# Performance work log

Hardware: AMD Instinct MI355X
Metric: run time of the kernel (lower is better)

The kernel has to match this reference:

```python
import jax, jax.numpy as jnp
import numpy as np
import math

B, S, D = 2, 2048, 1024
H, HKV = 16, 4
HD = D // H
NREP = H // HKV
E, TOPK, SHARED = 8, 2, 1
HIDDEN = 684
AUX_COEF = 0.01
RMS_EPS = 1e-5


def setup_inputs() -> dict:
    key = jax.random.key(0)
    ks = jax.random.split(key, 14)
    def w(k, shape):
        return jax.random.normal(k, shape, jnp.float32) * 0.02
    # standard RoPE angles, base 10000
    t = jnp.arange(S, dtype=jnp.float32)
    inv = 1.0 / (10000.0 ** (jnp.arange(0, HD, 2, dtype=jnp.float32) / HD))
    ang = t[:, None] * inv[None, :]  # [S, HD//2]
    return {
        "x": jax.random.normal(ks[0], (B, S, D), jnp.float32),
        "freqs_cos": jnp.cos(ang),
        "freqs_sin": jnp.sin(ang),
        "wq": w(ks[1], (D, D)),
        "wk": w(ks[2], (D, HKV * HD)),
        "wv": w(ks[3], (D, HKV * HD)),
        "wo": w(ks[4], (D, D)),
        "router_w": w(ks[5], (D, E)),
        "ew1": w(ks[6], (E, D, HIDDEN)),
        "ew2": w(ks[7], (E, HIDDEN, D)),
        "ew3": w(ks[8], (E, D, HIDDEN)),
        "sw1": w(ks[9], (SHARED, D, HIDDEN)),
        "sw2": w(ks[10], (SHARED, HIDDEN, D)),
        "sw3": w(ks[11], (SHARED, D, HIDDEN)),
        "g_attn": jnp.ones((D,), jnp.float32),
        "g_ffn": jnp.ones((D,), jnp.float32),
        "start_pos": 0,
    }


def rmsnorm(x, g, eps=RMS_EPS):
    xf = x.astype(jnp.float32)
    n = xf * jax.lax.rsqrt(jnp.mean(xf * xf, axis=-1, keepdims=True) + eps)
    return g * n.astype(x.dtype)


def rope(x, cos, sin):
    # pairs are consecutive elements (view_as_complex of reshape(..., -1, 2))
    xr, xi = x[..., 0::2], x[..., 1::2]
    c = cos[None, :, None, :]  # [1,S,1,HD//2]
    s = sin[None, :, None, :]
    r = xr * c - xi * s
    i = xr * s + xi * c
    return jnp.stack([r, i], axis=-1).reshape(x.shape)


def attention(x, freqs_cos, freqs_sin, wq, wk, wv, wo):
    b, s, d = x.shape
    q = (x @ wq).reshape(b, s, H, HD)
    k = (x @ wk).reshape(b, s, HKV, HD)
    v = (x @ wv).reshape(b, s, HKV, HD)
    q = rope(q, freqs_cos, freqs_sin)
    k = rope(k, freqs_cos, freqs_sin)
    k = jnp.repeat(k, NREP, axis=2)
    v = jnp.repeat(v, NREP, axis=2)
    q, k, v = (t.transpose(0, 2, 1, 3) for t in (q, k, v))  # [B,H,S,HD]
    att = jnp.einsum('bhqd,bhkd->bhqk', q, k) * (1.0 / math.sqrt(HD))
    # faithful to torch: tril then masked_fill(att == 0, -inf)
    tri = jnp.tril(jnp.ones((s, s), bool))
    att = jnp.where(tri, att, 0.0)
    att = jnp.where(att == 0.0, -jnp.inf, att)
    att = jax.nn.softmax(att, axis=-1)
    out = jnp.einsum('bhqk,bhkd->bhqd', att, v)
    out = out.transpose(0, 2, 1, 3).reshape(b, s, d)
    return out @ wo


def moe(x, router_w, ew1, ew2, ew3, sw1, sw2, sw3):
    b, s, d = x.shape
    xf = x.reshape(-1, d)                       # [N, D]
    logits = xf @ router_w                      # [N, E]
    probs = jax.nn.softmax(logits, axis=-1)
    _, topk_idx = jax.lax.top_k(logits, TOPK)   # [N, K]
    topk_p, _ = jax.lax.top_k(probs, TOPK)      # same ordering (softmax monotone)
    density = jnp.mean(jax.nn.one_hot(topk_idx[:, 0], E, dtype=jnp.float32), axis=0)
    aux = AUX_COEF * jnp.sum(density * jnp.mean(probs, axis=0)) * E
    # per-token combine weight over experts [N, E]
    onehot = jax.nn.one_hot(topk_idx, E, dtype=xf.dtype)  # [N, K, E]
    cw = jnp.einsum('nk,nke->ne', topk_p, onehot)
    # dense expert evaluation (jit-friendly dispatch/combine equivalent)
    h = jax.nn.silu(jnp.einsum('nd,edh->neh', xf, ew1)) * jnp.einsum('nd,edh->neh', xf, ew3)
    eo = jnp.einsum('neh,ehd->ned', h, ew2)
    out = jnp.einsum('ne,ned->nd', cw, eo)
    for i in range(SHARED):
        out = out + (jax.nn.silu(xf @ sw1[i]) * (xf @ sw3[i])) @ sw2[i]
    return out.reshape(b, s, d), aux


def reference(x, freqs_cos, freqs_sin, wq, wk, wv, wo, router_w, ew1, ew2, ew3, sw1, sw2, sw3, g_attn, g_ffn, start_pos):
    h = x + attention(rmsnorm(x, g_attn), freqs_cos, freqs_sin, wq, wk, wv, wo)
    ffn_out, aux = moe(rmsnorm(h, g_ffn), router_w, ew1, ew2, ew3, sw1, sw2, sw3)
    return h + ffn_out, aux
```

## Files before the change

kernel.cpp:

```cpp
#include <hip/hip_runtime.h>
#include <hip/hip_bf16.h>
#include <cstdint>

#define B_ 2
#define S_ 2048
#define D_ 1024
#define H_ 16
#define HKV_ 4
#define HD_ 64
#define E_ 8
#define HIDDEN_ 684
#define NT_ (B_*S_)
#define NEGBIG (-1e30f)

using bf16 = __hip_bfloat16;
typedef __attribute__((ext_vector_type(8))) short short8v;
typedef __attribute__((ext_vector_type(4))) short short4v;
typedef __attribute__((ext_vector_type(4))) float f32x4;

static __device__ __forceinline__ float b2f(bf16 v){ return __bfloat162float(v); }
static __device__ __forceinline__ bf16 f2b(float v){ return __float2bfloat16(v); }
static __device__ __forceinline__ short f2bs(float v){ bf16 h = f2b(v); return *reinterpret_cast<short*>(&h); }
static __device__ __forceinline__ float dload(const void* p, size_t i, int isbf){
  return isbf ? b2f(((const bf16*)p)[i]) : ((const float*)p)[i];
}

__global__ void k_detect(const uint32_t* __restrict__ g, int* __restrict__ flag, int* __restrict__ cnt){
  if(threadIdx.x == 0 && blockIdx.x == 0){
    uint32_t w0 = g[0], w1 = g[1], w2 = g[2], w3 = g[3];
    int bf;
    if(w0==0x3F803F80u && w1==0x3F803F80u && w2==0x3F803F80u && w3==0x3F803F80u) bf = 1;
    else if(w0==0x3F800000u && w1==0x3F800000u && w2==0x3F800000u && w3==0x3F800000u) bf = 0;
    else bf = 1;
    flag[0] = bf;
  }
  if(threadIdx.x < E_ && blockIdx.x == 0) cnt[threadIdx.x] = 0;
}

__global__ __launch_bounds__(256) void k_rms(const void* __restrict__ X, const void* __restrict__ g,
                                             bf16* __restrict__ outb, float* __restrict__ outf,
                                             const int* __restrict__ flag, int xdyn){
  int isbf = flag[0]; int xb = xdyn ? isbf : 0;
  int t = blockIdx.x; int tid = threadIdx.x;
  float v[4]; float ss = 0.f;
  #pragma unroll
  for(int i=0;i<4;i++){ v[i] = dload(X, (size_t)t*D_ + tid + i*256, xb); ss += v[i]*v[i]; }
  __shared__ float red[256];
  red[tid] = ss; __syncthreads();
  for(int st=128; st>0; st>>=1){ if(tid<st) red[tid] += red[tid+st]; __syncthreads(); }
  float r = rsqrtf(red[0]*(1.f/(float)D_) + 1e-5f);
  #pragma unroll
  for(int i=0;i<4;i++){
    int d = tid + i*256;
    float val = v[i]*r*dload(g, d, isbf);
    outb[(size_t)t*D_ + d] = f2b(val);
    if(outf) outf[(size_t)t*D_ + d] = val;
  }
}

#define ASTRIDE 40

static __device__ __forceinline__ f32x4 mfma16(short8v a, short8v b, f32x4 c){
  return __builtin_amdgcn_mfma_f32_16x16x32_bf16(a, b, c, 0, 0, 0);
}

template<int AMAP, int OMODE>
__global__ __launch_bounds__(256) void k_mgemm(
    const bf16* __restrict__ A, const void* __restrict__ Bw, void* __restrict__ Cout,
    const void* __restrict__ resid,
    int M, int N, int K, int ldc,
    const int* __restrict__ cnt, const int* __restrict__ offs, const int* __restrict__ list,
    const int* __restrict__ flag)
{
  int isbf = flag[0];
  int e, ct, rt;
  int base = 0; size_t eoff = 0;
  if(cnt){
    e = blockIdx.x;
    int nc = (N+63)>>6;
    ct = blockIdx.y % nc; rt = blockIdx.y / nc;
    M = cnt[e]; if(M<0) M=0; if(M>NT_) M=NT_;
    base = offs[e];
    eoff = (size_t)e*(size_t)K*(size_t)N;
  } else {
    e = 0; ct = blockIdx.x; rt = blockIdx.y;
  }
  int m0 = rt*128; if(m0 >= M) return;
  int n0 = ct*64;

  __shared__ short As[2][128*ASTRIDE];
  __shared__ short Bs[2][64*ASTRIDE];
  __shared__ int rowA[128];

  int tid = threadIdx.x;
  int w = tid>>6, l = tid&63, lr = l&15, lg = l>>4;

  if(tid < 128){
    int rloc = m0 + tid;
    int ar = -1;
    if(rloc < M) ar = (AMAP==2) ? (list[e*NT_ + rloc]>>1) : (base + rloc);
    rowA[tid] = ar;
  }
  __syncthreads();

  int srow = tid>>1, skh = (tid&1)*16;
  int keya = (srow>>4)&3, kb0 = skh>>3;
  int bk = tid>>3, bnc = (tid&7)*8;
  int keyb = ((tid&7)>>1)&3;
  int bcol = (((bk>>3)^keyb)<<3) + (bk&7);
  int arow = rowA[srow];

  short8v rA0, rA1, rB;

  auto loadAB = [&](int kt){
    int k0 = kt*32;
    {
      short tmp[16];
      if(arow >= 0 && k0+skh+16 <= K){
        const short4v* src = (const short4v*)(A + (size_t)arow*K + k0 + skh);
        #pragma unroll
        for(int c=0;c<4;c++) *(short4v*)&tmp[c*4] = src[c];
      } else {
        #pragma unroll
        for(int i=0;i<16;i++){
          int gk = k0+skh+i;
          short v = 0;
          if(arow>=0 && gk<K) v = *(const short*)&A[(size_t)arow*K+gk];
          tmp[i] = v;
        }
      }
      #pragma unroll
      for(int i=0;i<8;i++){ rA0[i]=tmp[i]; rA1[i]=tmp[8+i]; }
    }
    {
      int gk = k0 + bk;
      short tmp[8];
      if(gk < K && n0+bnc+8 <= N){
        size_t bb = eoff + (size_t)gk*N + n0 + bnc;
        if(isbf){
          const short4v* src = (const short4v*)((const bf16*)Bw + bb);
          *(short4v*)&tmp[0] = src[0];
          *(short4v*)&tmp[4] = src[1];
        } else {
          const f32x4* src = (const f32x4*)((const float*)Bw + bb);
          f32x4 f0 = src[0], f1 = src[1];
          #pragma unroll
          for(int i=0;i<4;i++){ tmp[i]=f2bs(f0[i]); tmp[4+i]=f2bs(f1[i]); }
        }
      } else {
        #pragma unroll
        for(int i=0;i<8;i++){
          int gn = n0+bnc+i;
          float v = 0.f;
          if(gk<K && gn<N) v = dload(Bw, eoff + (size_t)gk*N + gn, isbf);
          tmp[i] = f2bs(v);
        }
      }
      #pragma unroll
      for(int i=0;i<8;i++) rB[i]=tmp[i];
    }
  };
  auto writeAB = [&](int buf){
    *(short8v*)&As[buf][srow*ASTRIDE + ((kb0^keya)<<3)]     = rA0;
    *(short8v*)&As[buf][srow*ASTRIDE + (((kb0+1)^keya)<<3)] = rA1;
    #pragma unroll
    for(int i=0;i<8;i++) Bs[buf][(bnc+i)*ASTRIDE + bcol] = rB[i];
  };

  f32x4 acc[2][4] = {};
  int KT = (K+31)>>5;

  loadAB(0); writeAB(0);
  __syncthreads();
  int cur = 0;
  for(int kt=0; kt<KT; ++kt){
    bool more = (kt+1 < KT);
    if(more) loadAB(kt+1);
    short8v a[2], b[4];
    #pragma unroll
    for(int fi=0;fi<2;fi++)
      a[fi] = *(const short8v*)&As[cur][(w*32+fi*16+lr)*ASTRIDE + ((lg^((w*2+fi)&3))<<3)];
    #pragma unroll
    for(int fj=0;fj<4;fj++)
      b[fj] = *(const short8v*)&Bs[cur][(fj*16+lr)*ASTRIDE + ((lg^fj)<<3)];
    #pragma unroll
    for(int fi=0;fi<2;fi++)
      #pragma unroll
      for(int fj=0;fj<4;fj++)
        acc[fi][fj] = mfma16(a[fi], b[fj], acc[fi][fj]);
    if(more){ writeAB(cur^1); cur ^= 1; }
    __syncthreads();
  }

  #pragma unroll
  for(int fi=0;fi<2;fi++){
    #pragma unroll
    for(int r=0;r<4;r++){
      int rl = m0 + w*32 + fi*16 + lg*4 + r;
      if(rl >= M) continue;
      int orow;
      if(OMODE==2){ orow = list[e*NT_ + rl]; if(orow<0||orow>=2*NT_) continue; }
      else orow = base + rl;
      #pragma unroll
      for(int fj=0;fj<4;fj++){
        int gcol = n0 + fj*16 + lr;
        if(gcol >= N) continue;
        float v = acc[fi][fj][r];
        size_t o = (size_t)orow*ldc + gcol;
        if(OMODE==1)      ((float*)Cout)[o] = v + dload(resid, o, isbf);
        else if(OMODE==2) ((bf16*)Cout)[o] = f2b(v);
        else if(OMODE==3) ((float*)Cout)[o] = ((float*)Cout)[o] + v;
        else              ((bf16*)Cout)[o] = f2b(v);
      }
    }
  }
}

__global__ __launch_bounds__(256) void k_qkv(
    const bf16* __restrict__ A, const void* __restrict__ Wq, const void* __restrict__ Wk,
    const void* __restrict__ Wv, bf16* __restrict__ Oq, bf16* __restrict__ Ok, bf16* __restrict__ Ov,
    const void* __restrict__ fc, const void* __restrict__ fs,
    const int* __restrict__ flag)
{
  int isbf = flag[0];
  int ct = blockIdx.x, rt = blockIdx.y;
  const void* Bw; bf16* Cout; int N, n0;
  if(ct < 16){ Bw = Wq; Cout = Oq; N = D_;  n0 = ct*64; }
  else if(ct < 20){ Bw = Wk; Cout = Ok; N = 256; n0 = (ct-16)*64; }
  else { Bw = Wv; Cout = Ov; N = 256; n0 = (ct-20)*64; }
  const int K = D_, M = NT_;
  int m0 = rt*128;
  int dorope = (ct < 20);

  __shared__ short As[2][128*ASTRIDE];
  __shared__ short Bs[2][64*ASTRIDE];

  int tid = threadIdx.x;
  int w = tid>>6, l = tid&63, lr = l&15, lg = l>>4;

  int srow = tid>>1, skh = (tid&1)*16;
  int keya = (srow>>4)&3, kb0 = skh>>3;
  int bk = tid>>3, bnc = (tid&7)*8;
  int keyb = ((tid&7)>>1)&3;
  int bcol = (((bk>>3)^keyb)<<3) + (bk&7);
  int arow = m0 + srow;

  short8v rA0, rA1, rB;

  auto loadAB = [&](int kt){
    int k0 = kt*32;
    {
      short tmp[16];
      const short4v* src = (const short4v*)(A + (size_t)arow*K + k0 + skh);
      #pragma unroll
      for(int c=0;c<4;c++) *(short4v*)&tmp[c*4] = src[c];
      #pragma unroll
      for(int i=0;i<8;i++){ rA0[i]=tmp[i]; rA1[i]=tmp[8+i]; }
    }
    {
      int gk = k0 + bk;
      short tmp[8];
      size_t bb = (size_t)gk*N + n0 + bnc;
      if(isbf){
        const short4v* src = (const short4v*)((const bf16*)Bw + bb);
        *(short4v*)&tmp[0] = src[0];
        *(short4v*)&tmp[4] = src[1];
      } else {
        const f32x4* src = (const f32x4*)((const float*)Bw + bb);
        f32x4 f0 = src[0], f1 = src[1];
        #pragma unroll
        for(int i=0;i<4;i++){ tmp[i]=f2bs(f0[i]); tmp[4+i]=f2bs(f1[i]); }
      }
      #pragma unroll
      for(int i=0;i<8;i++) rB[i]=tmp[i];
    }
  };
  auto writeAB = [&](int buf){
    *(short8v*)&As[buf][srow*ASTRIDE + ((kb0^keya)<<3)]     = rA0;
    *(short8v*)&As[buf][srow*ASTRIDE + (((kb0+1)^keya)<<3)] = rA1;
    #pragma unroll
    for(int i=0;i<8;i++) Bs[buf][(bnc+i)*ASTRIDE + bcol] = rB[i];
  };

  f32x4 acc[2][4] = {};
  int KT = K>>5;

  loadAB(0); writeAB(0);
  __syncthreads();
  int cur = 0;
  for(int kt=0; kt<KT; ++kt){
    bool more = (kt+1 < KT);
    if(more) loadAB(kt+1);
    short8v a[2], b[4];
    #pragma unroll
    for(int fi=0;fi<2;fi++)
      a[fi] = *(const short8v*)&As[cur][(w*32+fi*16+lr)*ASTRIDE + ((lg^((w*2+fi)&3))<<3)];
    #pragma unroll
    for(int fj=0;fj<4;fj++)
      b[fj] = *(const short8v*)&Bs[cur][(fj*16+lr)*ASTRIDE + ((lg^fj)<<3)];
    #pragma unroll
    for(int fi=0;fi<2;fi++)
      #pragma unroll
      for(int fj=0;fj<4;fj++)
        acc[fi][fj] = mfma16(a[fi], b[fj], acc[fi][fj]);
    if(more){ writeAB(cur^1); cur ^= 1; }
    __syncthreads();
  }

  #pragma unroll
  for(int fi=0;fi<2;fi++){
    #pragma unroll
    for(int r=0;r<4;r++){
      int rl = m0 + w*32 + fi*16 + lg*4 + r;
      int s = rl & (S_-1);
      #pragma unroll
      for(int fj=0;fj<4;fj++){
        int gcol = n0 + fj*16 + lr;
        float v = acc[fi][fj][r];
        if(dorope){
          float partner = __shfl_xor(v, 1, 64);
          int p = (gcol & 63) >> 1;
          float c = dload(fc, s*32 + p, isbf);
          float sn = dload(fs, s*32 + p, isbf);
          if((l & 1) == 0) v = v*c - partner*sn;
          else             v = partner*sn + v*c;
        }
        Cout[(size_t)rl*N + gcol] = f2b(v);
      }
    }
  }
}

__global__ __launch_bounds__(256) void k_ffn1m(
    const bf16* __restrict__ A, const void* __restrict__ W1e, const void* __restrict__ W3e,
    const void* __restrict__ W1s, const void* __restrict__ W3s,
    bf16* __restrict__ OutE, bf16* __restrict__ OutS,
    const int* __restrict__ cnt, const int* __restrict__ offs, const int* __restrict__ list,
    const int* __restrict__ flag)
{
  int isbf = flag[0];
  const int K = D_, N = HIDDEN_;
  int e = blockIdx.x, y = blockIdx.y;
  int ct, rt, M, base, gat;
  const void* W1; const void* W3; bf16* Out;
  size_t eoff;
  if(y < 352){
    ct = y % 11; rt = y / 11;
    M = cnt[e]; if(M<0) M=0; if(M>NT_) M=NT_;
    base = offs[e]; gat = 1;
    W1 = W1e; W3 = W3e; Out = OutE;
    eoff = (size_t)e*(size_t)K*(size_t)N;
  } else {
    int ys = (y-352)*8 + e;
    ct = ys % 11; rt = ys / 11;
    M = NT_; base = 0; gat = 0;
    W1 = W1s; W3 = W3s; Out = OutS;
    eoff = 0;
  }
  int m0 = rt*128; if(m0 >= M) return;
  int n0 = ct*64;

  __shared__ short As[2][128*ASTRIDE];
  __shared__ short B1s[2][64*ASTRIDE];
  __shared__ short B3s[2][64*ASTRIDE];
  __shared__ int rowA[128];

  int tid = threadIdx.x;
  int w = tid>>6, l = tid&63, lr = l&15, lg = l>>4;

  if(tid < 128){
    int rloc = m0 + tid;
    int ar = -1;
    if(rloc < M) ar = gat ? (list[e*NT_ + rloc]>>1) : rloc;
    rowA[tid] = ar;
  }
  __syncthreads();

  int srow = tid>>1, skh = (tid&1)*16;
  int keya = (srow>>4)&3, kb0 = skh>>3;
  int bk = tid>>3, bnc = (tid&7)*8;
  int keyb = ((tid&7)>>1)&3;
  int bcol = (((bk>>3)^keyb)<<3) + (bk&7);
  int arow = rowA[srow];

  short8v rA0, rA1, rB1, rB3;

  auto loadB = [&](const void* Bw, int kt, short8v& rB){
    int k0 = kt*32;
    int gk = k0 + bk;
    short tmp[8];
    if(gk < K && n0+bnc+8 <= N){
      size_t bb = eoff + (size_t)gk*N + n0 + bnc;
      if(isbf){
        const short4v* src = (const short4v*)((const bf16*)Bw + bb);
        *(short4v*)&tmp[0] = src[0];
        *(short4v*)&tmp[4] = src[1];
      } else {
        const f32x4* src = (const f32x4*)((const float*)Bw + bb);
        f32x4 f0 = src[0], f1 = src[1];
        #pragma unroll
        for(int i=0;i<4;i++){ tmp[i]=f2bs(f0[i]); tmp[4+i]=f2bs(f1[i]); }
      }
    } else {
      #pragma unroll
      for(int i=0;i<8;i++){
        int gn = n0+bnc+i;
        float v = 0.f;
        if(gk<K && gn<N) v = dload(Bw, eoff + (size_t)gk*N + gn, isbf);
        tmp[i] = f2bs(v);
      }
    }
    #pragma unroll
    for(int i=0;i<8;i++) rB[i]=tmp[i];
  };
  auto loadA = [&](int kt){
    int k0 = kt*32;
    short tmp[16];
    if(arow >= 0 && k0+skh+16 <= K){
      const short4v* src = (const short4v*)(A + (size_t)arow*K + k0 + skh);
      #pragma unroll
      for(int c=0;c<4;c++) *(short4v*)&tmp[c*4] = src[c];
    } else {
      #pragma unroll
      for(int i=0;i<16;i++){
        int gk = k0+skh+i;
        short v = 0;
        if(arow>=0 && gk<K) v = *(const short*)&A[(size_t)arow*K+gk];
        tmp[i] = v;
      }
    }
    #pragma unroll
    for(int i=0;i<8;i++){ rA0[i]=tmp[i]; rA1[i]=tmp[8+i]; }
  };
  auto writeAll = [&](int buf){
    *(short8v*)&As[buf][srow*ASTRIDE + ((kb0^keya)<<3)]     = rA0;
    *(short8v*)&As[buf][srow*ASTRIDE + (((kb0+1)^keya)<<3)] = rA1;
    #pragma unroll
    for(int i=0;i<8;i++){
      B1s[buf][(bnc+i)*ASTRIDE + bcol] = rB1[i];
      B3s[buf][(bnc+i)*ASTRIDE + bcol] = rB3[i];
    }
  };

  f32x4 a1[2][4] = {}, a3[2][4] = {};
  int KT = (K+31)>>5;

  loadA(0); loadB(W1, 0, rB1); loadB(W3, 0, rB3); writeAll(0);
  __syncthreads();
  int cur = 0;
  for(int kt=0; kt<KT; ++kt){
    bool more = (kt+1 < KT);
    if(more){ loadA(kt+1); loadB(W1, kt+1, rB1); loadB(W3, kt+1, rB3); }
    short8v a[2], b1[4], b3[4];
    #pragma unroll
    for(int fi=0;fi<2;fi++)
      a[fi] = *(const short8v*)&As[cur][(w*32+fi*16+lr)*ASTRIDE + ((lg^((w*2+fi)&3))<<3)];
    #pragma unroll
    for(int fj=0;fj<4;fj++){
      b1[fj] = *(const short8v*)&B1s[cur][(fj*16+lr)*ASTRIDE + ((lg^fj)<<3)];
      b3[fj] = *(const short8v*)&B3s[cur][(fj*16+lr)*ASTRIDE + ((lg^fj)<<3)];
    }
    #pragma unroll
    for(int fi=0;fi<2;fi++)
      #pragma unroll
      for(int fj=0;fj<4;fj++){
        a1[fi][fj] = mfma16(a[fi], b1[fj], a1[fi][fj]);
        a3[fi][fj] = mfma16(a[fi], b3[fj], a3[fi][fj]);
      }
    if(more){ writeAll(cur^1); cur ^= 1; }
    __syncthreads();
  }

  #pragma unroll
  for(int fi=0;fi<2;fi++){
    #pragma unroll
    for(int r=0;r<4;r++){
      int rl = m0 + w*32 + fi*16 + lg*4 + r;
      if(rl >= M) continue;
      int orow = base + rl;
      #pragma unroll
      for(int fj=0;fj<4;fj++){
        int gcol = n0 + fj*16 + lr;
        if(gcol >= N) continue;
        float sg = a1[fi][fj][r];
        float v = (sg/(1.f+__expf(-sg))) * a3[fi][fj][r];
        Out[(size_t)orow*N + gcol] = f2b(v);
      }
    }
  }
}

__global__ __launch_bounds__(256) void k_ffn2m(
    const bf16* __restrict__ Ae, const bf16* __restrict__ Ash,
    const void* __restrict__ W2e, const void* __restrict__ W2s,
    bf16* __restrict__ OutE, float* __restrict__ OutS,
    const int* __restrict__ cnt, const int* __restrict__ offs, const int* __restrict__ list,
    const int* __restrict__ flag)
{
  int isbf = flag[0];
  const int K = HIDDEN_, N = D_;
  int e = blockIdx.x, y = blockIdx.y;
  int ct, rt, M, base, exm;
  const bf16* A; const void* Bw;
  size_t eoff;
  if(y < 512){
    ct = y % 16; rt = y / 16;
    M = cnt[e]; if(M<0) M=0; if(M>NT_) M=NT_;
    base = offs[e]; exm = 1;
    A = Ae; Bw = W2e;
    eoff = (size_t)e*(size_t)K*(size_t)N;
  } else {
    int ys = (y-512)*8 + e;
    ct = ys % 16; rt = ys / 16;
    M = NT_; base = 0; exm = 0;
    A = Ash; Bw = W2s;
    eoff = 0;
  }
  int m0 = rt*128; if(m0 >= M) return;
  int n0 = ct*64;

  __shared__ short As[2][128*ASTRIDE];
  __shared__ short Bs[2][64*ASTRIDE];

  int tid = threadIdx.x;
  int w = tid>>6, l = tid&63, lr = l&15, lg = l>>4;

  int srow = tid>>1, skh = (tid&1)*16;
  int keya = (srow>>4)&3, kb0 = skh>>3;
  int bk = tid>>3, bnc = (tid&7)*8;
  int keyb = ((tid&7)>>1)&3;
  int bcol = (((bk>>3)^keyb)<<3) + (bk&7);
  int arow = (m0 + srow < M) ? (base + m0 + srow) : -1;

  short8v rA0, rA1, rB;

  auto loadAB = [&](int kt){
    int k0 = kt*32;
    {
      short tmp[16];
      if(arow >= 0 && k0+skh+16 <= K){
        const short4v* src = (const short4v*)(A + (size_t)arow*K + k0 + skh);
        #pragma unroll
        for(int c=0;c<4;c++) *(short4v*)&tmp[c*4] = src[c];
      } else {
        #pragma unroll
        for(int i=0;i<16;i++){
          int gk = k0+skh+i;
          short v = 0;
          if(arow>=0 && gk<K) v = *(const short*)&A[(size_t)arow*K+gk];
          tmp[i] = v;
        }
      }
      #pragma unroll
      for(int i=0;i<8;i++){ rA0[i]=tmp[i]; rA1[i]=tmp[8+i]; }
    }
    {
      int gk = k0 + bk;
      short tmp[8];
      if(gk < K && n0+bnc+8 <= N){
        size_t bb = eoff + (size_t)gk*N + n0 + bnc;
        if(isbf){
          const short4v* src = (const short4v*)((const bf16*)Bw + bb);
          *(short4v*)&tmp[0] = src[0];
          *(short4v*)&tmp[4] = src[1];
        } else {
          const f32x4* src = (const f32x4*)((const float*)Bw + bb);
          f32x4 f0 = src[0], f1 = src[1];
          #pragma unroll
          for(int i=0;i<4;i++){ tmp[i]=f2bs(f0[i]); tmp[4+i]=f2bs(f1[i]); }
        }
      } else {
        #pragma unroll
        for(int i=0;i<8;i++){
          int gn = n0+bnc+i;
          float v = 0.f;
          if(gk<K && gn<N) v = dload(Bw, eoff + (size_t)gk*N + gn, isbf);
          tmp[i] = f2bs(v);
        }
      }
      #pragma unroll
      for(int i=0;i<8;i++) rB[i]=tmp[i];
    }
  };
  auto writeAB = [&](int buf){
    *(short8v*)&As[buf][srow*ASTRIDE + ((kb0^keya)<<3)]     = rA0;
    *(short8v*)&As[buf][srow*ASTRIDE + (((kb0+1)^keya)<<3)] = rA1;
    #pragma unroll
    for(int i=0;i<8;i++) Bs[buf][(bnc+i)*ASTRIDE + bcol] = rB[i];
  };

  f32x4 acc[2][4] = {};
  int KT = (K+31)>>5;

  loadAB(0); writeAB(0);
  __syncthreads();
  int cur = 0;
  for(int kt=0; kt<KT; ++kt){
    bool more = (kt+1 < KT);
    if(more) loadAB(kt+1);
    short8v a[2], b[4];
    #pragma unroll
    for(int fi=0;fi<2;fi++)
      a[fi] = *(const short8v*)&As[cur][(w*32+fi*16+lr)*ASTRIDE + ((lg^((w*2+fi)&3))<<3)];
    #pragma unroll
    for(int fj=0;fj<4;fj++)
      b[fj] = *(const short8v*)&Bs[cur][(fj*16+lr)*ASTRIDE + ((lg^fj)<<3)];
    #pragma unroll
    for(int fi=0;fi<2;fi++)
      #pragma unroll
      for(int fj=0;fj<4;fj++)
        acc[fi][fj] = mfma16(a[fi], b[fj], acc[fi][fj]);
    if(more){ writeAB(cur^1); cur ^= 1; }
    __syncthreads();
  }

  #pragma unroll
  for(int fi=0;fi<2;fi++){
    #pragma unroll
    for(int r=0;r<4;r++){
      int rl = m0 + w*32 + fi*16 + lg*4 + r;
      if(rl >= M) continue;
      if(exm){
        int orow = list[e*NT_ + rl];
        if(orow<0||orow>=2*NT_) continue;
        #pragma unroll
        for(int fj=0;fj<4;fj++){
          int gcol = n0 + fj*16 + lr;
          OutE[(size_t)orow*N + gcol] = f2b(acc[fi][fj][r]);
        }
      } else {
        #pragma unroll
        for(int fj=0;fj<4;fj++){
          int gcol = n0 + fj*16 + lr;
          size_t o = (size_t)rl*N + gcol;
          OutS[o] = OutS[o] + acc[fi][fj][r];
        }
      }
    }
  }
}

#define TST 72

__global__ __launch_bounds__(256) void k_attn(const bf16* __restrict__ Q, const bf16* __restrict__ Kg,
                                              const bf16* __restrict__ V, bf16* __restrict__ Out){
  int qt_ = (S_/64 - 1) - blockIdx.x;
  int h = blockIdx.y, b = blockIdx.z;
  int kvh = h>>2;
  const bf16* qb = Q + (size_t)b*S_*D_ + h*HD_;
  const bf16* kb = Kg + (size_t)b*S_*256 + kvh*HD_;
  const bf16* vb = V  + (size_t)b*S_*256 + kvh*HD_;
  __shared__ short Qs[64*TST];
  __shared__ short Ks[64*TST];
  __shared__ short Vt[64*TST];
  __shared__ short Ps[4][16*TST];
  int tid = threadIdx.x;
  int w = tid>>6, l = tid&63, lr = l&15, lg = l>>4;
  int sr = tid>>2, sc0 = (tid&3)*16;
  int vc = (((sr>>3)^(tid&3))<<3) + (sr&7);

  {
    const short8v* src = (const short8v*)(qb + (size_t)(qt_*64 + sr)*D_ + sc0);
    *(short8v*)&Qs[sr*TST + sc0]     = src[0];
    *(short8v*)&Qs[sr*TST + sc0 + 8] = src[1];
  }
  __syncthreads();
  short8v aQ0 = *(const short8v*)&Qs[(w*16+lr)*TST + lg*8];
  short8v aQ1 = *(const short8v*)&Qs[(w*16+lr)*TST + lg*8 + 32];

  float mreg[4], lreg[4];
  f32x4 accO[4] = {};
  #pragma unroll
  for(int r=0;r<4;r++){ mreg[r] = NEGBIG; lreg[r] = 0.f; }

  for(int kt=0; kt<=qt_; ++kt){
    __syncthreads();
    {
      const short8v* ksrc = (const short8v*)(kb + (size_t)(kt*64 + sr)*256 + sc0);
      *(short8v*)&Ks[sr*TST + sc0]     = ksrc[0];
      *(short8v*)&Ks[sr*TST + sc0 + 8] = ksrc[1];
      const short8v* vsrc = (const short8v*)(vb + (size_t)(kt*64 + sr)*256 + sc0);
      short8v v0 = vsrc[0], v1 = vsrc[1];
      #pragma unroll
      for(int i=0;i<8;i++){
        Vt[(sc0+i)*TST + vc]   = v0[i];
        Vt[(sc0+8+i)*TST + vc] = v1[i];
      }
    }
    __syncthreads();
    f32x4 s[4];
    #pragma unroll
    for(int fj=0; fj<4; fj++){
      short8v b0 = *(const short8v*)&Ks[(fj*16+lr)*TST + lg*8];
      short8v b1 = *(const short8v*)&Ks[(fj*16+lr)*TST + lg*8 + 32];
      f32x4 z = {};
      z = mfma16(aQ0, b0, z);
      z = mfma16(aQ1, b1, z);
      s[fj] = z;
    }
    #pragma unroll
    for(int fj=0; fj<4; fj++)
      #pragma unroll
      for(int r=0;r<4;r++){
        float v = s[fj][r]*0.125f;
        if(kt==qt_ && (fj*16+lr) > (w*16+lg*4+r)) v = NEGBIG;
        s[fj][r] = v;
      }
    float p[4][4], sc[4];
    #pragma unroll
    for(int r=0;r<4;r++){
      float mx = fmaxf(fmaxf(s[0][r],s[1][r]), fmaxf(s[2][r],s[3][r]));
      mx = fmaxf(mx, __shfl_xor(mx,1,64));
      mx = fmaxf(mx, __shfl_xor(mx,2,64));
      mx = fmaxf(mx, __shfl_xor(mx,4,64));
      mx = fmaxf(mx, __shfl_xor(mx,8,64));
      float mn = fmaxf(mreg[r], mx);
      sc[r] = __expf(mreg[r]-mn);
      float ps = 0.f;
      #pragma unroll
      for(int fj=0;fj<4;fj++){ float pv = __expf(s[fj][r]-mn); p[fj][r] = pv; ps += pv; }
      ps += __shfl_xor(ps,1,64); ps += __shfl_xor(ps,2,64);
      ps += __shfl_xor(ps,4,64); ps += __shfl_xor(ps,8,64);
      lreg[r] = lreg[r]*sc[r] + ps;
      mreg[r] = mn;
    }
    #pragma unroll
    for(int fj=0;fj<4;fj++)
      #pragma unroll
      for(int r=0;r<4;r++)
        accO[fj][r] *= sc[r];
    #pragma unroll
    for(int fj=0;fj<4;fj++)
      #pragma unroll
      for(int r=0;r<4;r++)
        Ps[w][(lg*4+r)*TST + fj*16+lr] = f2bs(p[fj][r]);
    short8v a0 = *(const short8v*)&Ps[w][lr*TST + lg*8];
    short8v a1 = *(const short8v*)&Ps[w][lr*TST + lg*8 + 32];
    #pragma unroll
    for(int fj=0;fj<4;fj++){
      int row = fj*16+lr;
      short8v b0 = *(const short8v*)&Vt[row*TST + ((lg^fj)<<3)];
      short8v b1 = *(const short8v*)&Vt[row*TST + (((lg^fj)+4)<<3)];
      accO[fj] = mfma16(a0, b0, accO[fj]);
      accO[fj] = mfma16(a1, b1, accO[fj]);
    }
  }
  #pragma unroll
  for(int r=0;r<4;r++){
    int qr = qt_*64 + w*16 + lg*4 + r;
    float inv = (lreg[r] > 0.f) ? 1.f/lreg[r] : 0.f;
    #pragma unroll
    for(int fj=0;fj<4;fj++)
      Out[((size_t)(b*S_+qr))*D_ + h*HD_ + fj*16+lr] = f2b(accO[fj][r]*inv);
  }
}

__global__ __launch_bounds__(64) void k_router(const float* __restrict__ X, const void* __restrict__ W,
                                               float* __restrict__ probs, float* __restrict__ p01,
                                               int* __restrict__ idx0buf, int* __restrict__ list,
                                               int* __restrict__ cnt, const int* __restrict__ flag){
  int isbf = flag[0];
  int t = blockIdx.x; int lane = threadIdx.x;
  float pe[8] = {};
  if(isbf){
    const bf16* Wb = (const bf16*)W;
    for(int d = lane; d < D_; d += 64){
      float xv = X[(size_t)t*D_ + d];
      #pragma unroll
      for(int e=0;e<8;e++) pe[e] += xv*b2f(Wb[(size_t)d*E_+e]);
    }
  } else {
    const float* Wf = (const float*)W;
    for(int d = lane; d < D_; d += 64){
      float xv = X[(size_t)t*D_ + d];
      #pragma unroll
      for(int e=0;e<8;e++) pe[e] += xv*Wf[(size_t)d*E_+e];
    }
  }
  for(int msk=1;msk<64;msk<<=1)
    #pragma unroll
    for(int e=0;e<8;e++) pe[e] += __shfl_xor(pe[e], msk, 64);
  if(lane == 0){
    float mx = pe[0];
    #pragma unroll
    for(int e=1;e<8;e++) mx = fmaxf(mx, pe[e]);
    float pr[8], sum = 0.f;
    #pragma unroll
    for(int e=0;e<8;e++){ pr[e] = __expf(pe[e]-mx); sum += pr[e]; }
    #pragma unroll
    for(int e=0;e<8;e++){ pr[e] /= sum; probs[t*8+e] = pr[e]; }
    int i0 = 0;
    #pragma unroll
    for(int e=1;e<8;e++) if(pe[e] > pe[i0]) i0 = e;
    int i1 = -1;
    #pragma unroll
    for(int e=0;e<8;e++){ if(e==i0) continue; if(i1<0 || pe[e] > pe[i1]) i1 = e; }
    p01[t*2]   = pr[i0];
    p01[t*2+1] = pr[i1];
    idx0buf[t] = i0;
    int pos = atomicAdd(&cnt[i0], 1);
    if(pos >= 0 && pos < NT_) list[i0*NT_ + pos] = t*2;
    pos     = atomicAdd(&cnt[i1], 1);
    if(pos >= 0 && pos < NT_) list[i1*NT_ + pos] = t*2 + 1;
  }
}

__global__ __launch_bounds__(256) void k_stats(const float* __restrict__ probs, const int* __restrict__ idx0buf,
                                               float* __restrict__ cnt0f, float* __restrict__ psum){
  int e = blockIdx.x; int tid = threadIdx.x;
  float sp = 0.f, sc = 0.f;
  for(int n = tid; n < NT_; n += 256){ sp += probs[n*8+e]; sc += (idx0buf[n]==e) ? 1.f : 0.f; }
  __shared__ float r1[256], r2[256];
  r1[tid] = sp; r2[tid] = sc; __syncthreads();
  for(int st=128; st>0; st>>=1){ if(tid<st){ r1[tid]+=r1[tid+st]; r2[tid]+=r2[tid+st]; } __syncthreads(); }
  if(tid==0){ psum[e] = r1[0]; cnt0f[e] = r2[0]; }
}

__global__ void k_finish(const float* __restrict__ cnt0f, const float* __restrict__ psum,
                         const int* __restrict__ cnt, int* __restrict__ offs,
                         bf16* __restrict__ auxb, float* __restrict__ auxf, const int* __restrict__ flag){
  if(threadIdx.x==0 && blockIdx.x==0){
    int o = 0;
    for(int e=0;e<8;e++){ offs[e] = o; int c = cnt[e]; if(c < 0) c = 0; if(c > NT_) c = NT_; o += c; }
    float aux = 0.f;
    for(int e=0;e<8;e++) aux += (cnt0f[e]*(1.f/(float)NT_))*(psum[e]*(1.f/(float)NT_));
    float v = aux*0.01f*8.f;
    if(flag[0]) auxb[0] = f2b(v); else auxf[0] = v;
  }
}

__global__ __launch_bounds__(256) void k_combine(const float* __restrict__ hbuf, const bf16* __restrict__ eosl,
                                                 const float* __restrict__ p01,
                                                 bf16* __restrict__ outb, float* __restrict__ outf,
                                                 const int* __restrict__ flag){
  int t = blockIdx.x; int tid = threadIdx.x;
  int isbf = flag[0];
  float p0 = p01[t*2], p1 = p01[t*2+1];
  #pragma unroll
  for(int i=0;i<4;i++){
    int d = tid + i*256;
    float v = hbuf[(size_t)t*D_ + d]
            + p0*b2f(eosl[((size_t)(t*2))*D_ + d])
            + p1*b2f(eosl[((size_t)(t*2+1))*D_ + d]);
    size_t o = (size_t)t*D_ + d;
    if(isbf) outb[o] = f2b(v); else outf[o] = v;
  }
}

static const size_t O_HBUF = 0;
static const size_t O_XNB  = 16777216;
static const size_t O_QLIN = 25165824;
static const size_t O_KLIN = 33554432;
static const size_t O_VLIN = 35651584;
static const size_t O_AOUT = 37748736;
static const size_t O_XN2B = 16777216;
static const size_t O_XN2F = 25165824;
static const size_t O_HEXP = 46137344;
static const size_t O_SHH  = 57344000;
static const size_t O_EOSL = 16777216;
static const size_t O_PROBS= 62947328;
static const size_t O_P01  = 63078400;
static const size_t O_IDX0 = 63111168;
static const size_t O_LIST = 63127552;
static const size_t O_CNT  = 63258624;
static const size_t O_CNT0 = 63258656;
static const size_t O_PSUM = 63258688;
static const size_t O_OFFS = 63258720;
static const size_t O_FLAG = 63258752;

extern "C" void kernel_launch(void* const* d_in, const int* in_sizes, int n_in,
                              void* d_out, int out_size, void* d_ws, size_t ws_size,
                              hipStream_t stream){
  (void)in_sizes; (void)n_in; (void)out_size; (void)ws_size;
  char* ws = (char*)d_ws;
  float* hbuf = (float*)(ws + O_HBUF);
  bf16* xnb   = (bf16*)(ws + O_XNB);
  bf16* qlin  = (bf16*)(ws + O_QLIN);
  bf16* klin  = (bf16*)(ws + O_KLIN);
  bf16* vlin  = (bf16*)(ws + O_VLIN);
  bf16* aout  = (bf16*)(ws + O_AOUT);
  bf16* xn2b  = (bf16*)(ws + O_XN2B);
  float* xn2f = (float*)(ws + O_XN2F);
  bf16* hexp  = (bf16*)(ws + O_HEXP);
  bf16* shh   = (bf16*)(ws + O_SHH);
  bf16* eosl  = (bf16*)(ws + O_EOSL);
  float* probs=(float*)(ws + O_PROBS);
  float* p01 = (float*)(ws + O_P01);
  int*  idx0 = (int*)(ws + O_IDX0);
  int*  list = (int*)(ws + O_LIST);
  int*  cnt  = (int*)(ws + O_CNT);
  float* cnt0f=(float*)(ws + O_CNT0);
  float* psum= (float*)(ws + O_PSUM);
  int*  offs = (int*)(ws + O_OFFS);
  int*  flg  = (int*)(ws + O_FLAG);

  bf16* outb = (bf16*)d_out;
  float* outf = (float*)d_out;
  bf16* auxb = outb + (size_t)NT_*D_;
  float* auxf = outf + (size_t)NT_*D_;

  k_detect<<<1, 64, 0, stream>>>((const uint32_t*)d_in[14], flg, cnt);

  k_rms<<<NT_, 256, 0, stream>>>(d_in[0], d_in[14], xnb, nullptr, flg, 1);

  k_qkv<<<dim3(24,32), 256, 0, stream>>>(xnb, d_in[3], d_in[4], d_in[5], qlin, klin, vlin,
                                         d_in[1], d_in[2], flg);

  k_attn<<<dim3(S_/64, H_, B_), 256, 0, stream>>>(qlin, klin, vlin, aout);

  k_mgemm<0,1><<<dim3(16,32), 256, 0, stream>>>(aout, d_in[6], hbuf, d_in[0], NT_, D_, D_, D_, nullptr, nullptr, nullptr, flg);

  k_rms<<<NT_, 256, 0, stream>>>(hbuf, d_in[15], xn2b, xn2f, flg, 0);

  k_router<<<NT_, 64, 0, stream>>>(xn2f, d_in[7], probs, p01, idx0, list, cnt, flg);
  k_stats<<<E_, 256, 0, stream>>>(probs, idx0, cnt0f, psum);
  k_finish<<<1, 64, 0, stream>>>(cnt0f, psum, cnt, offs, auxb, auxf, flg);

  k_ffn1m<<<dim3(E_, 352+44), 256, 0, stream>>>(xn2b, d_in[8], d_in[10], d_in[11], d_in[13],
                                                hexp, shh, cnt, offs, list, flg);

  k_ffn2m<<<dim3(E_, 512+64), 256, 0, stream>>>(hexp, shh, d_in[9], d_in[12],
                                                eosl, hbuf, cnt, offs, list, flg);

  k_combine<<<NT_, 256, 0, stream>>>(hbuf, eosl, p01, outb, outf, flg);
}
```

Before: 620.6 us.

## Widen FFN2 GEMM tile to 128 columns and drop LDS double buffering

The FFN down-projection kernel now covers 128 output columns per block instead of 64, doubling the accumulator tile and halving the grid. Each A tile loaded into shared memory is reused across twice as many MFMAs, which cuts global and LDS traffic for the activations. To fit the larger B tile, shared memory is single-buffered, which adds a second barrier per k-step and loses the overlap of LDS writes with compute. Register pressure from the larger accumulator and the smaller grid may lower occupancy.

```diff
diff --git a/kernel.cpp b/kernel.cpp
--- a/kernel.cpp
+++ b/kernel.cpp
@@ -503,36 +503,36 @@
   int ct, rt, M, base, exm;
   const bf16* A; const void* Bw;
   size_t eoff;
-  if(y < 512){
-    ct = y % 16; rt = y / 16;
+  if(y < 256){
+    ct = y % 8; rt = y / 8;
     M = cnt[e]; if(M<0) M=0; if(M>NT_) M=NT_;
     base = offs[e]; exm = 1;
     A = Ae; Bw = W2e;
     eoff = (size_t)e*(size_t)K*(size_t)N;
   } else {
-    int ys = (y-512)*8 + e;
-    ct = ys % 16; rt = ys / 16;
+    int ys = (y-256)*8 + e;
+    ct = ys % 8; rt = ys / 8;
     M = NT_; base = 0; exm = 0;
     A = Ash; Bw = W2s;
     eoff = 0;
   }
   int m0 = rt*128; if(m0 >= M) return;
-  int n0 = ct*64;
-
-  __shared__ short As[2][128*ASTRIDE];
-  __shared__ short Bs[2][64*ASTRIDE];
+  int n0 = ct*128;
+
+  __shared__ short As[128*ASTRIDE];
+  __shared__ short Bs[128*ASTRIDE];
 
   int tid = threadIdx.x;
   int w = tid>>6, l = tid&63, lr = l&15, lg = l>>4;
 
   int srow = tid>>1, skh = (tid&1)*16;
   int keya = (srow>>4)&3, kb0 = skh>>3;
-  int bk = tid>>3, bnc = (tid&7)*8;
-  int keyb = ((tid&7)>>1)&3;
+  int bk = tid>>3, bnc = (tid&7)*16;
+  int keyb = (tid&7)&3;
   int bcol = (((bk>>3)^keyb)<<3) + (bk&7);
   int arow = (m0 + srow < M) ? (base + m0 + srow) : -1;
 
-  short8v rA0, rA1, rB;
+  short8v rA0, rA1, rB0v, rB1v;
 
   auto loadAB = [&](int kt){
     int k0 = kt*32;
@@ -556,62 +556,61 @@
     }
     {
       int gk = k0 + bk;
-      short tmp[8];
-      if(gk < K && n0+bnc+8 <= N){
+      short tmp[16];
+      if(gk < K){
         size_t bb = eoff + (size_t)gk*N + n0 + bnc;
         if(isbf){
           const short4v* src = (const short4v*)((const bf16*)Bw + bb);
-          *(short4v*)&tmp[0] = src[0];
-          *(short4v*)&tmp[4] = src[1];
+          #pragma unroll
+          for(int c=0;c<4;c++) *(short4v*)&tmp[c*4] = src[c];
         } else {
           const f32x4* src = (const f32x4*)((const float*)Bw + bb);
-          f32x4 f0 = src[0], f1 = src[1];
           #pragma unroll
-          for(int i=0;i<4;i++){ tmp[i]=f2bs(f0[i]); tmp[4+i]=f2bs(f1[i]); }
+          for(int c=0;c<4;c++){
+            f32x4 f = src[c];
+            #pragma unroll
+            for(int i=0;i<4;i++) tmp[c*4+i] = f2bs(f[i]);
+          }
         }
       } else {
         #pragma unroll
-        for(int i=0;i<8;i++){
-          int gn = n0+bnc+i;
-          float v = 0.f;
-          if(gk<K && gn<N) v = dload(Bw, eoff + (size_t)gk*N + gn, isbf);
-          tmp[i] = f2bs(v);
-        }
-      }
-      #pragma unroll
-      for(int i=0;i<8;i++) rB[i]=tmp[i];
+        for(int i=0;i<16;i++) tmp[i] = 0;
+      }
+      #pragma unroll
+      for(int i=0;i<8;i++){ rB0v[i]=tmp[i]; rB1v[i]=tmp[8+i]; }
     }
   };
-  auto writeAB = [&](int buf){
-    *(short8v*)&As[buf][srow*ASTRIDE + ((kb0^keya)<<3)]     = rA0;
-    *(short8v*)&As[buf][srow*ASTRIDE + (((kb0+1)^keya)<<3)] = rA1;
-    #pragma unroll
-    for(int i=0;i<8;i++) Bs[buf][(bnc+i)*ASTRIDE + bcol] = rB[i];
+  auto writeAB = [&](){
+    *(short8v*)&As[srow*ASTRIDE + ((kb0^keya)<<3)]     = rA0;
+    *(short8v*)&As[srow*ASTRIDE + (((kb0+1)^keya)<<3)] = rA1;
+    #pragma unroll
+    for(int i=0;i<8;i++) Bs[(bnc+i)*ASTRIDE + bcol]   = rB0v[i];
+    #pragma unroll
+    for(int i=0;i<8;i++) Bs[(bnc+8+i)*ASTRIDE + bcol] = rB1v[i];
   };
 
-  f32x4 acc[2][4] = {};
+  f32x4 acc[2][8] = {};
   int KT = (K+31)>>5;
 
-  loadAB(0); writeAB(0);
+  loadAB(0); writeAB();
   __syncthreads();
-  int cur = 0;
   for(int kt=0; kt<KT; ++kt){
     bool more = (kt+1 < KT);
     if(more) loadAB(kt+1);
-    short8v a[2], b[4];
+    short8v a[2], b[8];
     #pragma unroll
     for(int fi=0;fi<2;fi++)
-      a[fi] = *(const short8v*)&As[cur][(w*32+fi*16+lr)*ASTRIDE + ((lg^((w*2+fi)&3))<<3)];
-    #pragma unroll
-    for(int fj=0;fj<4;fj++)
-      b[fj] = *(const short8v*)&Bs[cur][(fj*16+lr)*ASTRIDE + ((lg^fj)<<3)];
+      a[fi] = *(const short8v*)&As[(w*32+fi*16+lr)*ASTRIDE + ((lg^((w*2+fi)&3))<<3)];
+    #pragma unroll
+    for(int fj=0;fj<8;fj++)
+      b[fj] = *(const short8v*)&Bs[(fj*16+lr)*ASTRIDE + ((lg^(fj&3))<<3)];
     #pragma unroll
     for(int fi=0;fi<2;fi++)
       #pragma unroll
-      for(int fj=0;fj<4;fj++)
+      for(int fj=0;fj<8;fj++)
         acc[fi][fj] = mfma16(a[fi], b[fj], acc[fi][fj]);
-    if(more){ writeAB(cur^1); cur ^= 1; }
     __syncthreads();
+    if(more){ writeAB(); __syncthreads(); }
   }
 
   #pragma unroll
@@ -624,13 +623,13 @@
         int orow = list[e*NT_ + rl];
         if(orow<0||orow>=2*NT_) continue;
         #pragma unroll
-        for(int fj=0;fj<4;fj++){
+        for(int fj=0;fj<8;fj++){
           int gcol = n0 + fj*16 + lr;
           OutE[(size_t)orow*N + gcol] = f2b(acc[fi][fj][r]);
         }
       } else {
         #pragma unroll
-        for(int fj=0;fj<4;fj++){
+        for(int fj=0;fj<8;fj++){
           int gcol = n0 + fj*16 + lr;
           size_t o = (size_t)rl*N + gcol;
           OutS[o] = OutS[o] + acc[fi][fj][r];
@@ -919,7 +918,7 @@
   k_ffn1m<<<dim3(E_, 352+44), 256, 0, stream>>>(xn2b, d_in[8], d_in[10], d_in[11], d_in[13],
                                                 hexp, shh, cnt, offs, list, flg);
 
-  k_ffn2m<<<dim3(E_, 512+64), 256, 0, stream>>>(hexp, shh, d_in[9], d_in[12],
+  k_ffn2m<<<dim3(E_, 256+32), 256, 0, stream>>>(hexp, shh, d_in[9], d_in[12],
                                                 eosl, hbuf, cnt, offs, list, flg);
 
   k_combine<<<NT_, 256, 0, stream>>>(hbuf, eosl, p01, outb, outf, flg);
```

After: 617.2 us, median of 3. About the same (-0.5%).
